# Kernel optimization log

Measured on AMD Instinct MI355X. Metric: run time of the kernel, lower is better.

The kernel has to match this reference:

```python
import jax, jax.numpy as jnp
import numpy as np

EPS = 1e-5

def _layer_norm(x, w, b):
    mu = jnp.mean(x, axis=-1, keepdims=True)
    var = jnp.mean(jnp.square(x - mu), axis=-1, keepdims=True)
    return (x - mu) * jax.lax.rsqrt(var + EPS) * w + b

def setup_inputs() -> dict:
    key = jax.random.key(0)
    ks = jax.random.split(key, 8)
    B, S, D = 8, 2048, 1024
    image_features = jax.random.normal(ks[0], (B, S, D), dtype=jnp.float32)
    text_features = jax.random.normal(ks[1], (B, S, D), dtype=jnp.float32)
    ln_w = jnp.ones((D,), dtype=jnp.float32)
    ln_b = jnp.zeros((D,), dtype=jnp.float32)
    lim = 1.0 / np.sqrt(D)
    W_img = jax.random.uniform(ks[2], (D, D), minval=-lim, maxval=lim, dtype=jnp.float32)
    b_img = jax.random.uniform(ks[3], (D,), minval=-lim, maxval=lim, dtype=jnp.float32)
    W_txt = jax.random.uniform(ks[4], (D, D), minval=-lim, maxval=lim, dtype=jnp.float32)
    b_txt = jax.random.uniform(ks[5], (D,), minval=-lim, maxval=lim, dtype=jnp.float32)
    return {"image_features": image_features, "text_features": text_features,
            "ln_w": ln_w, "ln_b": ln_b, "W_img": W_img, "b_img": b_img,
            "W_txt": W_txt, "b_txt": b_txt}

def reference(image_features, text_features, ln_w, ln_b, W_img, b_img, W_txt, b_txt):
    D = image_features.shape[-1]
    scale = D ** (-0.5)
    image_norm = _layer_norm(image_features, ln_w, ln_b)
    text_norm = _layer_norm(text_features, ln_w, ln_b)
    # torch Linear: x @ W^T + b
    image_proj = jnp.einsum('bsd,ed->bse', image_norm, W_img) + b_img  # [B,Si,D]
    text_proj = jnp.einsum('btd,ed->bte', text_norm, W_txt) + b_txt    # [B,St,D]
    attn = jnp.einsum('bsd,btd->bst', image_proj, text_proj) * scale   # [B,Si,St]
    attn = jax.nn.softmax(attn, axis=-1)
    image_out = jnp.einsum('bst,btd->bsd', attn, text_proj)            # [B,Si,D]
    text_out = jnp.einsum('bst,bsd->btd', attn, image_proj)            # [B,St,D]
    return (image_out, text_out)
```

## Files before the change

### kernel.cpp

```cpp
#include <hip/hip_runtime.h>


#define DEV __device__ __forceinline__

typedef short s16x8 __attribute__((ext_vector_type(8)));
typedef float f32x4 __attribute__((ext_vector_type(4)));

DEV unsigned short f2bf(float f){
  unsigned u = __float_as_uint(f);
  u = (u + 0x7fffu + ((u >> 16) & 1u)) >> 16;
  return (unsigned short)u;
}
DEV float bf2f(unsigned short s){ return __uint_as_float(((unsigned)s) << 16); }

DEV void ldsload16(const void* g, void* l){
  __builtin_amdgcn_global_load_lds((const __attribute__((address_space(1))) void*)g,
                                   (__attribute__((address_space(3))) void*)l, 16, 0, 0);
}

__global__ __launch_bounds__(256) void k_cvt(const float* __restrict__ src,
                                             unsigned short* __restrict__ dst, int n4){
  int i = blockIdx.x * 256 + threadIdx.x;
  if (i < n4){
    float4 v = ((const float4*)src)[i];
    ushort4 o;
    o.x = f2bf(v.x); o.y = f2bf(v.y); o.z = f2bf(v.z); o.w = f2bf(v.w);
    ((ushort4*)dst)[i] = o;
  }
}

__global__ __launch_bounds__(256) void k_ln(const float* __restrict__ x,
                                            const float* __restrict__ w,
                                            const float* __restrict__ b,
                                            unsigned short* __restrict__ y){
  int row = blockIdx.x, tid = threadIdx.x;
  float4 v = ((const float4*)(x + (size_t)row * 1024))[tid];
  float s  = v.x + v.y + v.z + v.w;
  float s2 = v.x*v.x + v.y*v.y + v.z*v.z + v.w*v.w;
  #pragma unroll
  for (int o = 32; o > 0; o >>= 1){ s += __shfl_xor(s, o, 64); s2 += __shfl_xor(s2, o, 64); }
  __shared__ float sh[8];
  int wv = tid >> 6, ln = tid & 63;
  if (!ln){ sh[wv] = s; sh[4 + wv] = s2; }
  __syncthreads();
  s  = sh[0] + sh[1] + sh[2] + sh[3];
  s2 = sh[4] + sh[5] + sh[6] + sh[7];
  float mean = s * (1.f/1024.f);
  float var  = s2 * (1.f/1024.f) - mean * mean;
  float rstd = rsqrtf(var + 1e-5f);
  float4 w4 = ((const float4*)w)[tid];
  float4 b4 = ((const float4*)b)[tid];
  ushort4 o;
  o.x = f2bf((v.x-mean)*rstd*w4.x + b4.x);
  o.y = f2bf((v.y-mean)*rstd*w4.y + b4.y);
  o.z = f2bf((v.z-mean)*rstd*w4.z + b4.z);
  o.w = f2bf((v.w-mean)*rstd*w4.w + b4.w);
  ((ushort4*)(y + (size_t)row * 1024))[tid] = o;
}

#define STG(MAT, BASE, LD, T, H) do{                                              \
  ldsload16((BASE) + (size_t)(wave*16 + sfr) * (LD) + (T)*64 + (H)*32 + sq*8,     \
            &MAT[(T)&1][H][wave][0]);                                             \
  ldsload16((BASE) + (size_t)(wave*16 + 128 + sfr) * (LD) + (T)*64 + (H)*32 + sq*8,\
            &MAT[(T)&1][H][wave + 8][0]);                                         \
}while(0)

template<int OUT_BF16>
__global__ __launch_bounds__(512, 2) void k_gemm256(const unsigned short* __restrict__ A,
                                                    const unsigned short* __restrict__ Bt,
                                                    void* __restrict__ C,
                                                    const float* __restrict__ bias, float scale,
                                                    int K, int lda, int ldb, int ldc,
                                                    long sA, long sB, long sC,
                                                    int NBX, int NBY){
  __shared__ __align__(16) unsigned short As[2][2][16][512];
  __shared__ __align__(16) unsigned short Bs[2][2][16][512];
  int nwg = gridDim.x;
  int bid = blockIdx.x;
  int swz = (bid & 7) * (nwg >> 3) + (bid >> 3);
  int bx = swz % NBX; int rem = swz / NBX;
  int by = rem % NBY; int bz = rem / NBY;

  int tid = threadIdx.x, lane = tid & 63, wave = tid >> 6;
  int wm = wave >> 2, wn = wave & 3;
  int q = lane >> 4, fr = lane & 15;
  const unsigned short* Ab = A  + (size_t)bz * sA + (size_t)by * 256 * lda;
  const unsigned short* Bb = Bt + (size_t)bz * sB + (size_t)bx * 256 * ldb;
  int v   = (lane & 7) ^ ((lane >> 3) & 7);
  int sfr = 2 * (lane >> 3) + (v >> 2);
  int sq  = v & 3;
  int roff = ((fr >> 1) << 6) + (((q + ((fr & 1) << 2)) ^ ((fr >> 1) & 7)) << 3);
  int NT = K >> 6;

  f32x4 acc[8][4];
  #pragma unroll
  for (int m = 0; m < 8; ++m)
    #pragma unroll
    for (int n = 0; n < 4; ++n) acc[m][n] = f32x4{0.f, 0.f, 0.f, 0.f};

  STG(As, Ab, lda, 0, 0); STG(Bs, Bb, ldb, 0, 0);
  STG(As, Ab, lda, 0, 1); STG(Bs, Bb, ldb, 0, 1);
  STG(As, Ab, lda, 1, 0); STG(Bs, Bb, ldb, 1, 0);
  asm volatile("s_waitcnt vmcnt(8)" ::: "memory");
  asm volatile("s_barrier" ::: "memory");

  for (int t = 0; t < NT; ++t){
    const int buf = t & 1;
    s16x8 bfr[4];
    #pragma unroll
    for (int ph = 0; ph < 4; ++ph){
      const int kk = ph >> 1;
      const unsigned short* Ah = &As[buf][kk][0][0];
      const unsigned short* Bh = &Bs[buf][kk][0][0];
      s16x8 af[4];
      if ((ph & 1) == 0){
        #pragma unroll
        for (int n = 0; n < 4; ++n)  bfr[n] = *(const s16x8*)&Bh[(wn*4 + n)*512 + roff];
        #pragma unroll
        for (int mi = 0; mi < 4; ++mi) af[mi] = *(const s16x8*)&Ah[(wm*8 + mi)*512 + roff];
      } else {
        #pragma unroll
        for (int mi = 0; mi < 4; ++mi) af[mi] = *(const s16x8*)&Ah[(wm*8 + 4 + mi)*512 + roff];
      }
      if (ph == 0){ if (t + 1 < NT) STG(As, Ab, lda, t + 1, 1); }
      if (ph == 1){ if (t + 1 < NT) STG(Bs, Bb, ldb, t + 1, 1); }
      if (ph == 2){ if (t + 2 < NT) STG(As, Ab, lda, t + 2, 0); }
      if (ph == 3){ if (t + 2 < NT) STG(Bs, Bb, ldb, t + 2, 0); }
      asm volatile("s_barrier" ::: "memory");
      asm volatile("s_waitcnt lgkmcnt(0)" ::: "memory");
      __builtin_amdgcn_s_setprio(1);
      #pragma unroll
      for (int mi = 0; mi < 4; ++mi)
        #pragma unroll
        for (int n = 0; n < 4; ++n)
          acc[(ph&1)*4 + mi][n] = __builtin_amdgcn_mfma_f32_16x16x32_bf16(
              af[mi], bfr[n], acc[(ph&1)*4 + mi][n], 0, 0, 0);
      __builtin_amdgcn_s_setprio(0);
      if (ph & 1){
        if (t + 2 < NT) asm volatile("s_waitcnt vmcnt(8)" ::: "memory");
        else            asm volatile("s_waitcnt vmcnt(0)" ::: "memory");
      }
      asm volatile("s_barrier" ::: "memory");
    }
  }
  size_t cb = (size_t)bz * sC;
  int row0 = by*256 + wm*128 + q*4;
  int col0 = bx*256 + wn*64 + fr;
  #pragma unroll
  for (int m = 0; m < 8; ++m){
    #pragma unroll
    for (int n = 0; n < 4; ++n){
      int col = col0 + n*16;
      float bv = bias ? bias[col] : 0.f;
      #pragma unroll
      for (int j = 0; j < 4; ++j){
        int row = row0 + m*16 + j;
        float vv = acc[m][n][j] * scale + bv;
        if (OUT_BF16) ((unsigned short*)C)[cb + (size_t)row*ldc + col] = f2bf(vv);
        else          ((float*)C)[cb + (size_t)row*ldc + col] = vv;
      }
    }
  }
}

__global__ __launch_bounds__(256) void k_transpose(const unsigned short* __restrict__ src,
                                                   unsigned short* __restrict__ dst,
                                                   int R, int C, long sS, long sD){
  __shared__ __align__(16) unsigned short tile[64 * 64];
  int tid = threadIdx.x;
  const unsigned short* sb = src + (size_t)blockIdx.z * sS;
  unsigned short* db = dst + (size_t)blockIdx.z * sD;
  int r0 = blockIdx.y * 64, c0 = blockIdx.x * 64;
  #pragma unroll
  for (int i = 0; i < 2; ++i){
    int ci = i * 256 + tid;
    int row = ci >> 3, cch = ci & 7;
    int pos = cch ^ (row & 7) ^ (row >> 3);
    uint4 v = *(const uint4*)&sb[(size_t)(r0 + row) * C + c0 + cch * 8];
    *(uint4*)&tile[row * 64 + pos * 8] = v;
  }
  __syncthreads();
  int ocp = tid >> 3, og = tid & 7;
  int oc = ocp * 2;
  union { uint4 v; unsigned short us[8]; } o0, o1;
  #pragma unroll
  for (int k = 0; k < 8; ++k){
    int r = og * 8 + k;
    int pos = (oc >> 3) ^ (r & 7) ^ (r >> 3);
    unsigned pr = *(const unsigned*)&tile[r * 64 + pos * 8 + (oc & 7)];
    o0.us[k] = (unsigned short)(pr & 0xffffu);
    o1.us[k] = (unsigned short)(pr >> 16);
  }
  *(uint4*)&db[(size_t)(c0 + oc    ) * R + r0 + og * 8] = o0.v;
  *(uint4*)&db[(size_t)(c0 + oc + 1) * R + r0 + og * 8] = o1.v;
}

__global__ __launch_bounds__(256) void k_softmax(unsigned short* __restrict__ a){
  size_t row = blockIdx.x;
  unsigned short* p = a + row * 2048;
  int tid = threadIdx.x;
  union { uint4 v; unsigned short us[8]; } in, out;
  in.v = *(const uint4*)&p[tid * 8];
  float x[8];
  #pragma unroll
  for (int j = 0; j < 8; ++j) x[j] = bf2f(in.us[j]);
  float mx = x[0];
  #pragma unroll
  for (int j = 1; j < 8; ++j) mx = fmaxf(mx, x[j]);
  #pragma unroll
  for (int o = 32; o > 0; o >>= 1) mx = fmaxf(mx, __shfl_xor(mx, o, 64));
  __shared__ float sh[8];
  int wv = tid >> 6, ln = tid & 63;
  if (!ln) sh[wv] = mx;
  __syncthreads();
  mx = fmaxf(fmaxf(sh[0], sh[1]), fmaxf(sh[2], sh[3]));
  float sm = 0.f, e[8];
  #pragma unroll
  for (int j = 0; j < 8; ++j){ e[j] = __expf(x[j] - mx); sm += e[j]; }
  #pragma unroll
  for (int o = 32; o > 0; o >>= 1) sm += __shfl_xor(sm, o, 64);
  if (!ln) sh[4 + wv] = sm;
  __syncthreads();
  sm = sh[4] + sh[5] + sh[6] + sh[7];
  float inv = 1.f / sm;
  #pragma unroll
  for (int j = 0; j < 8; ++j) out.us[j] = f2bf(e[j] * inv);
  *(uint4*)&p[tid * 8] = out.v;
}

extern "C" void kernel_launch(void* const* d_in, const int* in_sizes, int n_in,
                              void* d_out, int out_size, void* d_ws, size_t ws_size,
                              hipStream_t stream) {
  const float* img  = (const float*)d_in[0];
  const float* txt  = (const float*)d_in[1];
  const float* lnw  = (const float*)d_in[2];
  const float* lnb  = (const float*)d_in[3];
  const float* Wimg = (const float*)d_in[4];
  const float* bimg = (const float*)d_in[5];
  const float* Wtxt = (const float*)d_in[6];
  const float* btxt = (const float*)d_in[7];
  float* out = (float*)d_out;

  char* ws = (char*)d_ws;
  unsigned short* R1 = (unsigned short*)ws;
  unsigned short* R2 = (unsigned short*)(ws + 67108864);
  unsigned short* WB = (unsigned short*)(ws + 134217728);
  unsigned short* R4 = (unsigned short*)(ws + 138412032);

  const long PB = 2097152;
  const long AB = 4194304;

  k_cvt<<<1024, 256, 0, stream>>>(Wimg, WB,           262144);
  k_cvt<<<1024, 256, 0, stream>>>(Wtxt, WB + 1048576, 262144);
  k_ln<<<16384, 256, 0, stream>>>(img, lnw, lnb, R1);
  k_ln<<<16384, 256, 0, stream>>>(txt, lnw, lnb, R1 + 16777216);
  k_gemm256<1><<<256, 512, 0, stream>>>(R1,            WB,           R2,            bimg, 1.f,
                                        1024, 1024, 1024, 1024, 0, 0, 0, 4, 64);
  k_gemm256<1><<<256, 512, 0, stream>>>(R1 + 16777216, WB + 1048576, R2 + 16777216, btxt, 1.f,
                                        1024, 1024, 1024, 1024, 0, 0, 0, 4, 64);
  dim3 gt(16, 32, 8);
  k_transpose<<<gt, 256, 0, stream>>>(R2,            R1,            2048, 1024, PB, PB);
  k_transpose<<<gt, 256, 0, stream>>>(R2 + 16777216, R1 + 16777216, 2048, 1024, PB, PB);
  k_gemm256<1><<<512, 512, 0, stream>>>(R2, R2 + 16777216, R4, nullptr, 0.03125f,
                                        1024, 1024, 1024, 2048, PB, PB, AB, 8, 8);
  k_softmax<<<16384, 256, 0, stream>>>(R4);
  dim3 gat(32, 32, 8);
  k_transpose<<<gat, 256, 0, stream>>>(R4, R2, 2048, 2048, AB, AB);
  k_gemm256<0><<<256, 512, 0, stream>>>(R4, R1 + 16777216, out, nullptr, 1.f,
                                        2048, 2048, 2048, 1024, AB, PB, PB, 4, 8);
  k_gemm256<0><<<256, 512, 0, stream>>>(R2, R1, out + 16777216, nullptr, 1.f,
                                        2048, 2048, 2048, 1024, AB, PB, PB, 4, 8);
}
```

Measured before the change: 422.7 us.

## Restructure GEMM main loop into triple-buffered LDS with register double-buffered fragments

The bf16 GEMM main loop now uses three LDS slots of 32-wide K tiles, replacing the two 64-wide buffers split into halves. It prefetches three tiles ahead and keeps two sets of register fragments, so LDS reads for the next tile are issued before the MFMAs of the current one. The aim is fewer barriers per K step and overlap of LDS reads with MFMA work, hiding global and LDS latency. The cost is more register pressure from the doubled fragment sets, which could reduce occupancy under launch_bounds(512,2). The loop also assumes NT is even.

```diff
diff --git a/kernel.cpp b/kernel.cpp
--- a/kernel.cpp
+++ b/kernel.cpp
@@ -58,11 +58,38 @@
   ((ushort4*)(y + (size_t)row * 1024))[tid] = o;
 }
 
-#define STG(MAT, BASE, LD, T, H) do{                                              \
-  ldsload16((BASE) + (size_t)(wave*16 + sfr) * (LD) + (T)*64 + (H)*32 + sq*8,     \
-            &MAT[(T)&1][H][wave][0]);                                             \
-  ldsload16((BASE) + (size_t)(wave*16 + 128 + sfr) * (LD) + (T)*64 + (H)*32 + sq*8,\
-            &MAT[(T)&1][H][wave + 8][0]);                                         \
+#define STG(MAT, BASE, LD, T, SL) do{                                             \
+  ldsload16((BASE) + (size_t)(wave*16 + sfr) * (LD) + (T)*32 + sq*8,              \
+            &MAT[SL][wave][0]);                                                   \
+  ldsload16((BASE) + (size_t)(wave*16 + 128 + sfr) * (LD) + (T)*32 + sq*8,        \
+            &MAT[SL][wave + 8][0]);                                               \
+}while(0)
+
+#define STEP(T, FA_C, FB_C, FA_N, FB_N) do{                                       \
+  const int t_ = (T);                                                             \
+  if (t_ + 3 < NT){ const int sl = (t_) % 3;                                      \
+    STG(As, Ab, lda, t_ + 3, sl); STG(Bs, Bb, ldb, t_ + 3, sl); }                 \
+  if (t_ + 1 < NT){ const int sl = (t_ + 1) % 3;                                  \
+    const unsigned short* Ah = &As[sl][0][0];                                     \
+    const unsigned short* Bh = &Bs[sl][0][0];                                     \
+    _Pragma("unroll")                                                             \
+    for (int mi = 0; mi < 8; ++mi)                                                \
+      FA_N[mi] = *(const s16x8*)&Ah[(wm*8 + mi)*512 + roff];                      \
+    _Pragma("unroll")                                                             \
+    for (int n = 0; n < 4; ++n)                                                   \
+      FB_N[n] = *(const s16x8*)&Bh[(wn*4 + n)*512 + roff];                        \
+  }                                                                               \
+  __builtin_amdgcn_s_setprio(1);                                                  \
+  _Pragma("unroll")                                                               \
+  for (int mi = 0; mi < 8; ++mi)                                                  \
+    _Pragma("unroll")                                                             \
+    for (int n = 0; n < 4; ++n)                                                   \
+      acc[mi][n] = __builtin_amdgcn_mfma_f32_16x16x32_bf16(                       \
+          FA_C[mi], FB_C[n], acc[mi][n], 0, 0, 0);                                \
+  __builtin_amdgcn_s_setprio(0);                                                  \
+  if (t_ + 3 < NT) asm volatile("s_waitcnt vmcnt(4) lgkmcnt(0)" ::: "memory");    \
+  else             asm volatile("s_waitcnt vmcnt(0) lgkmcnt(0)" ::: "memory");    \
+  asm volatile("s_barrier" ::: "memory");                                         \
 }while(0)
 
 template<int OUT_BF16>
@@ -73,8 +100,8 @@
                                                     int K, int lda, int ldb, int ldc,
                                                     long sA, long sB, long sC,
                                                     int NBX, int NBY){
-  __shared__ __align__(16) unsigned short As[2][2][16][512];
-  __shared__ __align__(16) unsigned short Bs[2][2][16][512];
+  __shared__ __align__(16) unsigned short As[3][16][512];
+  __shared__ __align__(16) unsigned short Bs[3][16][512];
   int nwg = gridDim.x;
   int bid = blockIdx.x;
   int swz = (bid & 7) * (nwg >> 3) + (bid >> 3);
@@ -90,7 +117,7 @@
   int sfr = 2 * (lane >> 3) + (v >> 2);
   int sq  = v & 3;
   int roff = ((fr >> 1) << 6) + (((q + ((fr & 1) << 2)) ^ ((fr >> 1) & 7)) << 3);
-  int NT = K >> 6;
+  const int NT = K >> 5;
 
   f32x4 acc[8][4];
   #pragma unroll
@@ -98,51 +125,25 @@
     #pragma unroll
     for (int n = 0; n < 4; ++n) acc[m][n] = f32x4{0.f, 0.f, 0.f, 0.f};
 
+  s16x8 fa0[8], fb0[4], fa1[8], fb1[4];
+
   STG(As, Ab, lda, 0, 0); STG(Bs, Bb, ldb, 0, 0);
-  STG(As, Ab, lda, 0, 1); STG(Bs, Bb, ldb, 0, 1);
-  STG(As, Ab, lda, 1, 0); STG(Bs, Bb, ldb, 1, 0);
+  STG(As, Ab, lda, 1, 1); STG(Bs, Bb, ldb, 1, 1);
+  STG(As, Ab, lda, 2, 2); STG(Bs, Bb, ldb, 2, 2);
   asm volatile("s_waitcnt vmcnt(8)" ::: "memory");
   asm volatile("s_barrier" ::: "memory");
-
-  for (int t = 0; t < NT; ++t){
-    const int buf = t & 1;
-    s16x8 bfr[4];
-    #pragma unroll
-    for (int ph = 0; ph < 4; ++ph){
-      const int kk = ph >> 1;
-      const unsigned short* Ah = &As[buf][kk][0][0];
-      const unsigned short* Bh = &Bs[buf][kk][0][0];
-      s16x8 af[4];
-      if ((ph & 1) == 0){
-        #pragma unroll
-        for (int n = 0; n < 4; ++n)  bfr[n] = *(const s16x8*)&Bh[(wn*4 + n)*512 + roff];
-        #pragma unroll
-        for (int mi = 0; mi < 4; ++mi) af[mi] = *(const s16x8*)&Ah[(wm*8 + mi)*512 + roff];
-      } else {
-        #pragma unroll
-        for (int mi = 0; mi < 4; ++mi) af[mi] = *(const s16x8*)&Ah[(wm*8 + 4 + mi)*512 + roff];
-      }
-      if (ph == 0){ if (t + 1 < NT) STG(As, Ab, lda, t + 1, 1); }
-      if (ph == 1){ if (t + 1 < NT) STG(Bs, Bb, ldb, t + 1, 1); }
-      if (ph == 2){ if (t + 2 < NT) STG(As, Ab, lda, t + 2, 0); }
-      if (ph == 3){ if (t + 2 < NT) STG(Bs, Bb, ldb, t + 2, 0); }
-      asm volatile("s_barrier" ::: "memory");
-      asm volatile("s_waitcnt lgkmcnt(0)" ::: "memory");
-      __builtin_amdgcn_s_setprio(1);
-      #pragma unroll
-      for (int mi = 0; mi < 4; ++mi)
-        #pragma unroll
-        for (int n = 0; n < 4; ++n)
-          acc[(ph&1)*4 + mi][n] = __builtin_amdgcn_mfma_f32_16x16x32_bf16(
-              af[mi], bfr[n], acc[(ph&1)*4 + mi][n], 0, 0, 0);
-      __builtin_amdgcn_s_setprio(0);
-      if (ph & 1){
-        if (t + 2 < NT) asm volatile("s_waitcnt vmcnt(8)" ::: "memory");
-        else            asm volatile("s_waitcnt vmcnt(0)" ::: "memory");
-      }
-      asm volatile("s_barrier" ::: "memory");
-    }
-  }
+  #pragma unroll
+  for (int mi = 0; mi < 8; ++mi) fa0[mi] = *(const s16x8*)&As[0][wm*8 + mi][roff];
+  #pragma unroll
+  for (int n = 0; n < 4; ++n)    fb0[n]  = *(const s16x8*)&Bs[0][wn*4 + n][roff];
+  asm volatile("s_waitcnt lgkmcnt(0)" ::: "memory");
+  asm volatile("s_barrier" ::: "memory");
+
+  for (int t = 0; t < NT; t += 2){
+    STEP(t,     fa0, fb0, fa1, fb1);
+    STEP(t + 1, fa1, fb1, fa0, fb0);
+  }
+
   size_t cb = (size_t)bz * sC;
   int row0 = by*256 + wm*128 + q*4;
   int col0 = bx*256 + wn*64 + fr;
```

Result: slower. 481.2 us (+13.8%).
